# Kernel optimization log

Measured on AMD Instinct MI355X. Metric: run time of the kernel, lower is better.

## Reference

```python
import jax, jax.numpy as jnp
import numpy as np

B, N, T, L, H = 8, 128, 256, 32, 128


def setup_inputs() -> dict:
    key = jax.random.key(0)
    k0, k1, k2, k3, k4, k5 = jax.random.split(key, 6)
    x = jax.random.uniform(k0, (B, N, T), dtype=jnp.float32)
    s = 1.0 / np.sqrt(H)  # pytorch LSTM/Linear default init scale
    W_ih = jax.random.uniform(k1, (N, 4 * H, L), minval=-s, maxval=s, dtype=jnp.float32)
    b_ih = jax.random.uniform(k2, (N, 4 * H), minval=-s, maxval=s, dtype=jnp.float32)
    b_hh = jax.random.uniform(k3, (N, 4 * H), minval=-s, maxval=s, dtype=jnp.float32)
    W_fc = jax.random.uniform(k4, (N, N, H), minval=-s, maxval=s, dtype=jnp.float32)  # [node_i, out_j, H]
    b_fc = jax.random.uniform(k5, (N, N), minval=-s, maxval=s, dtype=jnp.float32)  # [node_i, out_j]
    return {"x": x, "W_ih": W_ih, "b_ih": b_ih, "b_hh": b_hh, "W_fc": W_fc, "b_fc": b_fc}


def reference(x, W_ih, b_ih, b_hh, W_fc, b_fc):
    # x: [B, N, T]
    Bn, Nn, Tn = x.shape
    Ln = W_ih.shape[-1]
    Hh = W_fc.shape[-1]
    Ttau = Tn - Ln  # number of prediction steps (t = L .. T-1)

    # Sliding windows x[:, i, tau:tau+L] for tau = 0..Ttau-1  -> [B, N, Ttau, L]
    idx = jnp.arange(Ttau)[:, None] + jnp.arange(Ln)[None, :]  # [Ttau, L]
    xw = x[:, :, idx]

    # Single-step LSTM with zero initial state: W_hh term vanishes.
    gates = jnp.einsum('bntl,ngl->bntg', xw, W_ih) + (b_ih + b_hh)[None, :, None, :]
    gi, gf, gg, go = jnp.split(gates, 4, axis=-1)  # pytorch order: i, f, g, o
    c = jax.nn.sigmoid(gi) * jnp.tanh(gg)          # f*c0 = 0
    h = jax.nn.sigmoid(go) * jnp.tanh(c)           # [B, N, Ttau, H]

    # Per-node fc (grouped GEMM): contributions[b, tau, j, i]
    contrib = jnp.einsum('bnth,njh->btjn', h, W_fc) + b_fc.T[None, None, :, :]

    # G[b, j, i] = mean_tau contrib[b, tau, j, i] / x[b, i, L + tau]
    denom = jnp.transpose(x[:, :, Ln:], (0, 2, 1))[:, :, None, :]  # [B, Ttau, 1, N_i]
    G = jnp.mean(contrib / denom, axis=1)                          # [B, N, N]

    X_hat = jnp.sum(contrib, axis=2) + 1e-6  # [B, Ttau, N]
    return G, X_hat
```

## Files before the change

### kernel.cpp

```cpp
#include <hip/hip_runtime.h>
#include <math.h>

#define B_  8
#define N_  128
#define T_  256
#define L_  32
#define H_  128
#define TT_ 224

typedef float f2    __attribute__((ext_vector_type(2)));
typedef float f4    __attribute__((ext_vector_type(4)));
typedef float f32x4 __attribute__((ext_vector_type(4)));
typedef short bf16x8 __attribute__((ext_vector_type(8)));

#define L2E_  1.4426950408889634f
#define L2E2_ 2.8853900817779268f

__device__ __forceinline__ unsigned pk2bf(float a, float b) {
    unsigned ua = __float_as_uint(a), ub = __float_as_uint(b);
    ua = (ua + 0x7FFFu + ((ua >> 16) & 1u)) >> 16;
    ub = (ub + 0x7FFFu + ((ub >> 16) & 1u)) >> 16;
    return ua | (ub << 16);
}
__device__ __forceinline__ float aexp2(float x) {
    float r; asm("v_exp_f32 %0, %1" : "=v"(r) : "v"(x)); return r;
}
__device__ __forceinline__ float aexp2n(float x) {
    float r; asm("v_exp_f32 %0, -%1" : "=v"(r) : "v"(x)); return r;
}
__device__ __forceinline__ float arcp(float x) {
    return __builtin_amdgcn_rcpf(x);
}

__global__ __launch_bounds__(512, 4)
void k_main(const float* __restrict__ x,
            const float* __restrict__ W_ih,
            const float* __restrict__ b_ih, const float* __restrict__ b_hh,
            const float* __restrict__ W_fc, const float* __restrict__ b_fc,
            float* __restrict__ G, float* __restrict__ xhat) {
    const int n   = blockIdx.x;
    const int y   = blockIdx.y;
    const int b0  = 2 * y;
    const int tid = threadIdx.x;
    const int w    = tid >> 6;
    const int lane = tid & 63;
    const int col  = lane & 15;
    const int quad = lane >> 4;

    __shared__ __attribute__((aligned(16))) float xs[2][260];
    __shared__ __attribute__((aligned(16))) unsigned xeo[2][2][128];
    __shared__ __attribute__((aligned(16))) float xr[2][TT_];
    __shared__ __attribute__((aligned(16))) float xh_part[2][8][TT_];
    __shared__ __attribute__((aligned(16))) float hd_loc[2][H_];
    __shared__ float red[8];
    __shared__ f4 wpart[16][32];
    __shared__ f4 ws4[32];
    __shared__ float bp[2];
    __shared__ float bs_s;

    union { uint4 u; bf16x8 v; } bfr[3];
    f32x4 biaR[3];
    {
        const int ht = w;
        const int hb = ht * 16 + quad * 4;
        #pragma unroll
        for (int g = 0; g < 3; ++g) {
            const int r  = g * 128 + ht * 16 + col;
            const int sr = r + (r >= 128 ? 128 : 0);
            const float sc = (g == 1) ? L2E2_ : L2E_;
            const f4* src = (const f4*)(W_ih + (size_t)n * 512 * L_ +
                                        (size_t)sr * L_ + quad * 8);
            f4 v0 = src[0] * sc, v1 = src[1] * sc;
            bfr[g].u.x = pk2bf(v0.x, v0.y);
            bfr[g].u.y = pk2bf(v0.z, v0.w);
            bfr[g].u.z = pk2bf(v1.x, v1.y);
            bfr[g].u.w = pk2bf(v1.z, v1.w);
            const int sg = (g == 0) ? 0 : (g == 1 ? 256 : 384);
            const f4 bi = *(const f4*)&b_ih[(size_t)n * 512 + sg + hb];
            const f4 bh = *(const f4*)&b_hh[(size_t)n * 512 + sg + hb];
            const f4 bs = (bi + bh) * sc;
            biaR[g][0] = bs.x; biaR[g][1] = bs.y;
            biaR[g][2] = bs.z; biaR[g][3] = bs.w;
        }
    }
    {
        const int h4 = tid & 31, jg = tid >> 5;
        const f4* Wf = (const f4*)(W_fc + (size_t)n * N_ * H_) +
                       (size_t)jg * 8 * 32 + h4;
        f4 s = {0.f, 0.f, 0.f, 0.f};
        #pragma unroll
        for (int j = 0; j < 8; ++j) s += Wf[j * 32];
        wpart[jg][h4] = s;
    }
    if (tid < 128) {
        float bv = b_fc[n * N_ + tid];
        #pragma unroll
        for (int off = 32; off > 0; off >>= 1) bv += __shfl_down(bv, off, 64);
        if ((tid & 63) == 0) bp[tid >> 6] = bv;
    }
    if (tid < 256) xs[0][tid] = x[((size_t)b0 * N_ + n) * T_ + tid];
    else           xs[1][tid - 256] = x[((size_t)(b0 + 1) * N_ + n) * T_ + (tid - 256)];
    if (tid < 4) { xs[0][256 + tid] = 0.f; xs[1][256 + tid] = 0.f; }
    __syncthreads();

    if (tid < TT_)                          xr[0][tid]       = 1.0f / xs[0][L_ + tid];
    else if (tid >= 256 && tid < 256 + TT_) xr[1][tid - 256] = 1.0f / xs[1][L_ + tid - 256];
    if (tid < 128) {
        xeo[0][0][tid] = pk2bf(xs[0][2 * tid],     xs[0][2 * tid + 1]);
        xeo[0][1][tid] = pk2bf(xs[0][2 * tid + 1], xs[0][2 * tid + 2]);
    } else if (tid >= 256 && tid < 384) {
        const int t2 = tid - 256;
        xeo[1][0][t2] = pk2bf(xs[1][2 * t2],     xs[1][2 * t2 + 1]);
        xeo[1][1][t2] = pk2bf(xs[1][2 * t2 + 1], xs[1][2 * t2 + 2]);
    }
    if (tid < 32) {
        f4 s = wpart[0][tid];
        #pragma unroll
        for (int jg = 1; jg < 16; ++jg) s += wpart[jg][tid];
        ws4[tid] = s;
    }
    if (tid == 0) bs_s = bp[0] + bp[1];
    __syncthreads();

    const f4 wshF = ws4[(w * 16 + quad * 4) >> 2];
    const float bsum_n = bs_s;

    const f32x4 zero4 = {0.f, 0.f, 0.f, 0.f};
    const int p    = (col + quad * 8) & 1;
    const int base = (col + quad * 8) >> 1;

    #pragma unroll
    for (int bb = 0; bb < 2; ++bb) {
        f32x4 hdacc = {0.f, 0.f, 0.f, 0.f};
        #pragma unroll
        for (int ttile = 0; ttile < 14; ++ttile) {
            union { uint4 u; bf16x8 v; } af;
            af.u.x = xeo[bb][p][ttile * 8 + base + 0];
            af.u.y = xeo[bb][p][ttile * 8 + base + 1];
            af.u.z = xeo[bb][p][ttile * 8 + base + 2];
            af.u.w = xeo[bb][p][ttile * 8 + base + 3];
            const float xrt = xr[bb][ttile * 16 + col];

            f32x4 gi = __builtin_amdgcn_mfma_f32_16x16x32_bf16(bfr[0].v, af.v, zero4, 0, 0, 0);
            f32x4 gg = __builtin_amdgcn_mfma_f32_16x16x32_bf16(bfr[1].v, af.v, zero4, 0, 0, 0);
            f32x4 go = __builtin_amdgcn_mfma_f32_16x16x32_bf16(bfr[2].v, af.v, zero4, 0, 0, 0);
            gi += biaR[0];
            gg += biaR[1];
            go += biaR[2];

            f32x4 e1, e2, e3;
            #pragma unroll
            for (int r = 0; r < 4; ++r) {
                e1[r] = aexp2n(gi[r]);
                e2[r] = aexp2(gg[r]);
                e3[r] = aexp2n(go[r]);
            }
            const f32x4 A  = (1.f + e1) * (e2 + 1.f);
            const f32x4 Bv = 1.f + e3;
            const f32x4 AB = A * Bv;
            f32x4 R;
            #pragma unroll
            for (int r = 0; r < 4; ++r) R[r] = arcp(AB[r]);
            const f32x4 em = e2 - 1.f;
            const f32x4 t  = em * R;
            const f32x4 c  = t * Bv;
            const f32x4 c2 = c * c;
            f32x4 Q = c2 * -0.027698f + 0.120833f;
            Q = c2 * Q - 0.331541f;
            Q = c2 * Q + 1.0f;
            const f32x4 hh = t * Q;

            hdacc += hh * xrt;
            float xsum = fmaf(hh[0], wshF.x,
                         fmaf(hh[1], wshF.y,
                         fmaf(hh[2], wshF.z,
                         fmaf(hh[3], wshF.w, 0.f))));
            xsum += __shfl_xor(xsum, 16, 64);
            xsum += __shfl_xor(xsum, 32, 64);
            if (lane < 16) xh_part[bb][w][ttile * 16 + lane] = xsum;
        }
        #pragma unroll
        for (int r = 0; r < 4; ++r) {
            float v = hdacc[r];
            v += __shfl_xor(v, 1, 64);
            v += __shfl_xor(v, 2, 64);
            v += __shfl_xor(v, 4, 64);
            v += __shfl_xor(v, 8, 64);
            if (col == 0) hd_loc[bb][w * 16 + quad * 4 + r] = v;
        }
    }

    {
        const int bb = w >> 2;
        const int t2 = tid - bb * 256;
        float dv = (t2 < TT_) ? xr[bb][t2] : 0.f;
        #pragma unroll
        for (int off = 32; off > 0; off >>= 1) dv += __shfl_down(dv, off, 64);
        if (lane == 0) red[w] = dv;
    }
    __syncthreads();

    {
        const int bb = tid >> 8;
        const int tt = tid & 255;
        if (tt < TT_) {
            const float v = (xh_part[bb][0][tt] + xh_part[bb][1][tt]) +
                            (xh_part[bb][2][tt] + xh_part[bb][3][tt]) +
                            (xh_part[bb][4][tt] + xh_part[bb][5][tt]) +
                            (xh_part[bb][6][tt] + xh_part[bb][7][tt]);
            xhat[((size_t)(b0 + bb) * TT_ + tt) * N_ + n] = v + bsum_n + 1e-6f;
        }
    }

    {
        const float dinv0 = (red[0] + red[1]) + (red[2] + red[3]);
        const float dinv1 = (red[4] + red[5]) + (red[6] + red[7]);
        const int j   = tid >> 2;
        const int qtr = tid & 3;
        const f4* Wf = (const f4*)(W_fc + ((size_t)n * N_ + j) * H_ + qtr * 32);
        float s0 = 0.f, s1 = 0.f;
        #pragma unroll
        for (int q = 0; q < 8; ++q) {
            const f4 wv = Wf[q];
            const int hb = qtr * 32 + q * 4;
            s0 = fmaf(wv.x, hd_loc[0][hb + 0],
                 fmaf(wv.y, hd_loc[0][hb + 1],
                 fmaf(wv.z, hd_loc[0][hb + 2],
                 fmaf(wv.w, hd_loc[0][hb + 3], s0))));
            s1 = fmaf(wv.x, hd_loc[1][hb + 0],
                 fmaf(wv.y, hd_loc[1][hb + 1],
                 fmaf(wv.z, hd_loc[1][hb + 2],
                 fmaf(wv.w, hd_loc[1][hb + 3], s1))));
        }
        s0 += __shfl_xor(s0, 1, 64);
        s0 += __shfl_xor(s0, 2, 64);
        s1 += __shfl_xor(s1, 1, 64);
        s1 += __shfl_xor(s1, 2, 64);
        if (qtr == 0) {
            const float bj = b_fc[n * N_ + j];
            G[(size_t)b0 * N_ * N_ + (size_t)j * N_ + n] =
                (s0 + bj * dinv0) * (1.0f / 224.0f);
            G[(size_t)(b0 + 1) * N_ * N_ + (size_t)j * N_ + n] =
                (s1 + bj * dinv1) * (1.0f / 224.0f);
        }
    }
}

extern "C" void kernel_launch(void* const* d_in, const int* in_sizes, int n_in,
                              void* d_out, int out_size, void* d_ws, size_t ws_size,
                              hipStream_t stream) {
    const float* x    = (const float*)d_in[0];
    const float* W_ih = (const float*)d_in[1];
    const float* b_ih = (const float*)d_in[2];
    const float* b_hh = (const float*)d_in[3];
    const float* W_fc = (const float*)d_in[4];
    const float* b_fc = (const float*)d_in[5];

    float* G    = (float*)d_out;
    float* xhat = (float*)d_out + (size_t)B_ * N_ * N_;

    (void)d_ws; (void)ws_size;

    k_main<<<dim3(N_, B_ / 2), dim3(512), 0, stream>>>(x, W_ih, b_ih, b_hh,
                                                       W_fc, b_fc, G, xhat);
}
```

Baseline: 105.6 us.

## Write outputs node-major to workspace and transpose with a separate kernel

The main kernel now writes G and X_hat in node-major order into a workspace, so each block's stores are contiguous instead of strided by N. A second small kernel transposes both buffers through shared memory into the required output layouts. This removes uncoalesced scattered stores but adds an extra launch and a full extra read and write of the outputs.

Result: no change. 106.7 us (+1.1%).

```diff
diff --git a/kernel.cpp b/kernel.cpp
--- a/kernel.cpp
+++ b/kernel.cpp
@@ -37,7 +37,7 @@
             const float* __restrict__ W_ih,
             const float* __restrict__ b_ih, const float* __restrict__ b_hh,
             const float* __restrict__ W_fc, const float* __restrict__ b_fc,
-            float* __restrict__ G, float* __restrict__ xhat) {
+            float* __restrict__ g_t, float* __restrict__ xh_t) {
     const int n   = blockIdx.x;
     const int y   = blockIdx.y;
     const int b0  = 2 * y;
@@ -208,7 +208,7 @@
                             (xh_part[bb][2][tt] + xh_part[bb][3][tt]) +
                             (xh_part[bb][4][tt] + xh_part[bb][5][tt]) +
                             (xh_part[bb][6][tt] + xh_part[bb][7][tt]);
-            xhat[((size_t)(b0 + bb) * TT_ + tt) * N_ + n] = v + bsum_n + 1e-6f;
+            xh_t[((size_t)n * B_ + (b0 + bb)) * TT_ + tt] = v + bsum_n + 1e-6f;
         }
     }
 
@@ -238,11 +238,46 @@
         s1 += __shfl_xor(s1, 2, 64);
         if (qtr == 0) {
             const float bj = b_fc[n * N_ + j];
-            G[(size_t)b0 * N_ * N_ + (size_t)j * N_ + n] =
+            g_t[((size_t)n * B_ + b0) * N_ + j] =
                 (s0 + bj * dinv0) * (1.0f / 224.0f);
-            G[(size_t)(b0 + 1) * N_ * N_ + (size_t)j * N_ + n] =
+            g_t[((size_t)n * B_ + b0 + 1) * N_ + j] =
                 (s1 + bj * dinv1) * (1.0f / 224.0f);
         }
+    }
+}
+
+__global__ __launch_bounds__(256)
+void k_tr(const float* __restrict__ xh_t, const float* __restrict__ g_t,
+          float* __restrict__ G, float* __restrict__ xhat) {
+    __shared__ float tile[32][129];
+    const int bid = blockIdx.x;
+    const int tid = threadIdx.x;
+    int b, c0, M;
+    const float* sbase;
+    float* dbase;
+    if (bid < 56) {
+        b = bid / 7; c0 = (bid % 7) * 32; M = TT_;
+        sbase = xh_t; dbase = xhat;
+    } else {
+        const int k = bid - 56;
+        b = k / 4; c0 = (k % 4) * 32; M = N_;
+        sbase = g_t; dbase = G;
+    }
+    const float* src = sbase + (size_t)b * M + c0;
+    float* dst = dbase + ((size_t)b * M + c0) * N_;
+
+    const int tl = tid & 31, nr = tid >> 5;
+    #pragma unroll
+    for (int ps = 0; ps < 16; ++ps) {
+        const int nn = ps * 8 + nr;
+        tile[tl][nn] = src[(size_t)nn * B_ * M + tl];
+    }
+    __syncthreads();
+    const int no = tid & 127, tr = tid >> 7;
+    #pragma unroll
+    for (int ps = 0; ps < 16; ++ps) {
+        const int tt = ps * 2 + tr;
+        dst[(size_t)tt * N_ + no] = tile[tt][no];
     }
 }
 
@@ -259,8 +294,10 @@
     float* G    = (float*)d_out;
     float* xhat = (float*)d_out + (size_t)B_ * N_ * N_;
 
-    (void)d_ws; (void)ws_size;
+    float* xh_t = (float*)d_ws;
+    float* g_t  = (float*)d_ws + (size_t)N_ * B_ * TT_;
 
     k_main<<<dim3(N_, B_ / 2), dim3(512), 0, stream>>>(x, W_ih, b_ih, b_hh,
-                                                       W_fc, b_fc, G, xhat);
-}
+                                                       W_fc, b_fc, g_t, xh_t);
+    k_tr<<<dim3(88), dim3(256), 0, stream>>>(xh_t, g_t, G, xhat);
+}
```
